# Optimization experiments

Measured on AMD Instinct MI355X. Metric: run time of the kernel, lower is better.

The kernel has to match this reference:

```python
import math
import jax, jax.numpy as jnp
import numpy as np

B, H, T, D = 4, 16, 1024, 64


def setup_inputs() -> dict:
    key0 = jax.random.key(0)
    ks = jax.random.split(key0, 5)
    return {
        "query": jax.random.normal(ks[0], (B, H, T, D), dtype=jnp.float32),
        "key": jax.random.normal(ks[1], (B, H, T, D), dtype=jnp.float32),
        "value": jax.random.normal(ks[2], (B, H, T, D), dtype=jnp.float32),
        "edges_key": jax.random.normal(ks[3], (T, T, D), dtype=jnp.float32),
        "edges_value": jax.random.normal(ks[4], (T, T, D), dtype=jnp.float32),
        "mask": jnp.ones((B, 1, 1, T), dtype=bool),
    }


def reference(query, key, value, edges_key, edges_value, mask):
    d = query.shape[-1]
    # content-content scores [B,H,T,T]
    scores = jnp.einsum("bhqd,bhkd->bhqk", query, key)
    # content-position scores via relative edge keys [T,T,D]
    scores = scores + jnp.einsum("bhqd,qkd->bhqk", query, edges_key)
    scores = scores * (1.0 / math.sqrt(d))
    scores = jnp.where(mask, scores, jnp.float32(-1e9))
    a = jax.nn.softmax(scores, axis=-1)  # dropout is identity in eval / pdrop=0
    # value update + relative edge-value update
    out = jnp.einsum("bhqk,bhkd->bhqd", a, value)
    out = out + jnp.einsum("bhqk,qkd->bhqd", a, edges_value)
    return out
```

## Files before the change

### kernel.cpp

```cpp
#include <hip/hip_runtime.h>

#define Tt 1024
#define Dh 64
#define SCALE 0.125f

typedef __attribute__((ext_vector_type(4))) float f32x4;
typedef __attribute__((ext_vector_type(8))) short bf16x8;

__device__ inline unsigned short f2bf(float x){
  unsigned u = __float_as_uint(x);
  unsigned r = (u + 0x7FFFu + ((u >> 16) & 1u)) >> 16;
  return (unsigned short)r;
}
__device__ inline float bf2f(unsigned short h){
  return __uint_as_float(((unsigned)h) << 16);
}
__device__ inline ushort4 pack4(float4 f){
  ushort4 u; u.x=f2bf(f.x); u.y=f2bf(f.y); u.z=f2bf(f.z); u.w=f2bf(f.w); return u;
}
__device__ inline bf16x8 pack8(float4 a, float4 b){
  bf16x8 r;
  r[0]=(short)f2bf(a.x); r[1]=(short)f2bf(a.y); r[2]=(short)f2bf(a.z); r[3]=(short)f2bf(a.w);
  r[4]=(short)f2bf(b.x); r[5]=(short)f2bf(b.y); r[6]=(short)f2bf(b.z); r[7]=(short)f2bf(b.w);
  return r;
}
__device__ inline f32x4 mfma16(bf16x8 a, bf16x8 b, f32x4 c){
  return __builtin_amdgcn_mfma_f32_16x16x32_bf16(a, b, c, 0, 0, 0);
}

__device__ inline void stage64x64(const float* __restrict__ g, unsigned short (*lds)[68], int tid){
  int r = tid >> 2, c = (tid & 3) * 16;
  const float4* g4 = (const float4*)(g + (size_t)r * 64 + c);
  float4 f0 = g4[0], f1 = g4[1], f2_ = g4[2], f3 = g4[3];
  ushort4* d4 = (ushort4*)&lds[r][c];
  d4[0]=pack4(f0); d4[1]=pack4(f1); d4[2]=pack4(f2_); d4[3]=pack4(f3);
}
__device__ inline void stage64x64T4(const float* __restrict__ g, unsigned short (*lds)[68], int tid){
  const int kb = (tid >> 4) * 4, db = (tid & 15) * 4;
  float fv[4][4];
#pragma unroll
  for (int j = 0; j < 4; ++j){
    float4 f = *(const float4*)(g + (size_t)(kb + j) * 64 + db);
    fv[j][0]=f.x; fv[j][1]=f.y; fv[j][2]=f.z; fv[j][3]=f.w;
  }
#pragma unroll
  for (int i = 0; i < 4; ++i){
    ushort4 u;
    u.x=f2bf(fv[0][i]); u.y=f2bf(fv[1][i]); u.z=f2bf(fv[2][i]); u.w=f2bf(fv[3][i]);
    *(ushort4*)&lds[db + i][kb] = u;
  }
}
__device__ inline void stage_rows(const unsigned short* __restrict__ g, size_t rowstride,
                                  unsigned short (*lds)[68], int tid){
  int r = tid >> 2, c = (tid & 3) * 16;
  const ushort4* s4 = (const ushort4*)(g + (size_t)r * rowstride + c);
  ushort4 u0=s4[0], u1=s4[1], u2=s4[2], u3=s4[3];
  ushort4* d4 = (ushort4*)&lds[r][c];
  d4[0]=u0; d4[1]=u1; d4[2]=u2; d4[3]=u3;
}
__device__ inline bf16x8 ldsfrag(const unsigned short (*lds)[68], int row, int col){
  const ushort4* p = (const ushort4*)&lds[row][col];
  ushort4 u0 = p[0], u1 = p[1];
  bf16x8 r;
  r[0]=(short)u0.x; r[1]=(short)u0.y; r[2]=(short)u0.z; r[3]=(short)u0.w;
  r[4]=(short)u1.x; r[5]=(short)u1.y; r[6]=(short)u1.z; r[7]=(short)u1.w;
  return r;
}
__device__ inline float fragsum(bf16x8 v){
  float s = 0.f;
#pragma unroll
  for (int i = 0; i < 8; ++i) s += bf2f((unsigned short)v[i]);
  return s;
}

__global__ __launch_bounds__(256) void k_qek(const float* __restrict__ Q,
                                             const float* __restrict__ EK,
                                             unsigned short* __restrict__ BIAS){
  __shared__ unsigned short ek[2][64][68];
  __shared__ unsigned short ot[4][16][68];
  const int qi = blockIdx.x;
  const int tid = threadIdx.x;
  const int w = tid >> 6, l = tid & 63, lr = l & 15, lg = l >> 4;

  bf16x8 a0, a1;
  {
    const float4* q4 = (const float4*)(Q + ((size_t)(16*w + lr) * Tt + qi) * Dh);
    a0 = pack8(q4[lg*2],     q4[lg*2 + 1]);
    a1 = pack8(q4[8 + lg*2], q4[8 + lg*2 + 1]);
  }
  const float* ekq = EK + (size_t)qi * Tt * Dh;
  const int r = l >> 2, c2 = (l & 3) * 16;
  unsigned short* dst0 = BIAS + (size_t)(16*w + r) * Tt * Tt + (size_t)qi * Tt + c2;

  stage64x64(ekq, ek[0], tid);
  __syncthreads();

  for (int kt = 0; kt < 16; ++kt){
    if (kt < 15) stage64x64(ekq + (size_t)(kt+1) * 64 * Dh, ek[(kt+1)&1], tid);
    const unsigned short (*cur)[68] = ek[kt&1];
    f32x4 acc[4];
#pragma unroll
    for (int c = 0; c < 4; ++c){
      bf16x8 b0 = ldsfrag(cur, c*16 + lr, lg*8);
      bf16x8 b1 = ldsfrag(cur, c*16 + lr, lg*8 + 32);
      f32x4 z = {0.f,0.f,0.f,0.f};
      z = mfma16(a0, b0, z);
      z = mfma16(a1, b1, z);
      acc[c] = z;
    }
#pragma unroll
    for (int c = 0; c < 4; ++c)
#pragma unroll
      for (int j = 0; j < 4; ++j)
        ot[w][lg*4 + j][c*16 + lr] = f2bf(acc[c][j]);
    __builtin_amdgcn_wave_barrier();
    {
      const ushort4* s4 = (const ushort4*)&ot[w][r][c2];
      ushort4 u0=s4[0], u1=s4[1], u2=s4[2], u3=s4[3];
      ushort4* d4 = (ushort4*)(dst0 + kt*64);
      d4[0]=u0; d4[1]=u1; d4[2]=u2; d4[3]=u3;
    }
    __builtin_amdgcn_wave_barrier();
    __syncthreads();
  }
}

__global__ __launch_bounds__(256) void k_attn(const float* __restrict__ Q,
                                              const float* __restrict__ K,
                                              const float* __restrict__ V,
                                              unsigned short* WS,
                                              float* __restrict__ OUT){
  __shared__ unsigned short kt_[64][68];
  __shared__ unsigned short bt[64][68];
  __shared__ unsigned short pt[64][68];
  __shared__ unsigned short vt[64][68];
  const int bid = blockIdx.x;
  const int bh = (bid & 7) + ((bid >> 7) << 3);
  const int qt = ((bid >> 3) & 15) * 64;
  const int tid = threadIdx.x;
  const int w = tid >> 6, l = tid & 63, lr = l & 15, lg = l >> 4;

  bf16x8 a0, a1;
  {
    const float4* q4 = (const float4*)(Q + ((size_t)bh * Tt + qt + 16*w + lr) * Dh);
    a0 = pack8(q4[lg*2],     q4[lg*2 + 1]);
    a1 = pack8(q4[8 + lg*2], q4[8 + lg*2 + 1]);
  }
  const float* kb = K + (size_t)bh * Tt * Dh;
  const float* vb = V + (size_t)bh * Tt * Dh;
  unsigned short* wsb = WS + (size_t)bh * Tt * Tt;

  float lsum[4] = {0.f,0.f,0.f,0.f};
  f32x4 oacc[4];
#pragma unroll
  for (int c = 0; c < 4; ++c) oacc[c] = (f32x4){0.f,0.f,0.f,0.f};

  for (int kt = 0; kt < 16; ++kt){
    stage64x64(kb + (size_t)kt * 64 * Dh, kt_, tid);
    stage_rows(wsb + (size_t)qt * Tt + kt*64, Tt, bt, tid);
    stage64x64T4(vb + (size_t)kt * 64 * Dh, vt, tid);
    __syncthreads();
#pragma unroll
    for (int c = 0; c < 4; ++c){
      bf16x8 b0 = ldsfrag(kt_, c*16 + lr, lg*8);
      bf16x8 b1 = ldsfrag(kt_, c*16 + lr, lg*8 + 32);
      f32x4 z = {0.f,0.f,0.f,0.f};
      z = mfma16(a0, b0, z);
      z = mfma16(a1, b1, z);
      int kl = c*16 + lr;
#pragma unroll
      for (int j = 0; j < 4; ++j){
        float s = (z[j] + bf2f(bt[16*w + lg*4 + j][kl])) * SCALE;
        float p = __expf(s);
        lsum[j] += p;
        pt[16*w + lg*4 + j][kl] = f2bf(p);
      }
    }
    __syncthreads();
    {
      int r = tid >> 2, c2 = (tid & 3) * 16;
      const ushort4* s4 = (const ushort4*)&pt[r][c2];
      ushort4 u0=s4[0], u1=s4[1], u2=s4[2], u3=s4[3];
      ushort4* d4 = (ushort4*)(wsb + (size_t)(qt + r) * Tt + kt*64 + c2);
      d4[0]=u0; d4[1]=u1; d4[2]=u2; d4[3]=u3;
    }
    bf16x8 p0 = ldsfrag(pt, 16*w + lr, lg*8);
    bf16x8 p1 = ldsfrag(pt, 16*w + lr, lg*8 + 32);
#pragma unroll
    for (int c = 0; c < 4; ++c){
      bf16x8 v0 = ldsfrag(vt, c*16 + lr, lg*8);
      bf16x8 v1 = ldsfrag(vt, c*16 + lr, lg*8 + 32);
      oacc[c] = mfma16(p0, v0, oacc[c]);
      oacc[c] = mfma16(p1, v1, oacc[c]);
    }
    __syncthreads();
  }
  float rl[4];
#pragma unroll
  for (int j = 0; j < 4; ++j){
    float su = lsum[j];
    for (int o = 1; o < 16; o <<= 1) su += __shfl_xor(su, o, 64);
    rl[j] = 1.f / su;
  }
#pragma unroll
  for (int c = 0; c < 4; ++c)
#pragma unroll
    for (int j = 0; j < 4; ++j)
      OUT[((size_t)bh * Tt + qt + 16*w + lg*4 + j) * Dh + c*16 + lr] = oacc[c][j] * rl[j];
}

__global__ __launch_bounds__(256) void k_aev(const unsigned short* __restrict__ WS,
                                             const float* __restrict__ EV,
                                             float* __restrict__ OUT){
  __shared__ unsigned short evt[2][64][68];
  __shared__ float sums[64];
  const int qi = blockIdx.x;
  const int tid = threadIdx.x;
  const int w = tid >> 6, l = tid & 63, lr = l & 15, lg = l >> 4;

  const unsigned short* arow = WS + (size_t)(16*w + lr) * Tt * Tt + (size_t)qi * Tt;
  const float* evq = EV + (size_t)qi * Tt * Dh;

  f32x4 acc[4];
#pragma unroll
  for (int c = 0; c < 4; ++c) acc[c] = (f32x4){0.f,0.f,0.f,0.f};
  float asum = 0.f;

  stage64x64T4(evq, evt[0], tid);
  __syncthreads();

  for (int kt = 0; kt < 16; ++kt){
    if (kt < 15) stage64x64T4(evq + (size_t)(kt+1) * 64 * Dh, evt[(kt+1)&1], tid);
    const unsigned short (*cur)[68] = evt[kt&1];
    bf16x8 a0 = *(const bf16x8*)(arow + kt*64 + lg*8);
    bf16x8 a1 = *(const bf16x8*)(arow + kt*64 + 32 + lg*8);
    asum += fragsum(a0) + fragsum(a1);
#pragma unroll
    for (int c = 0; c < 4; ++c){
      bf16x8 b0 = ldsfrag(cur, c*16 + lr, lg*8);
      bf16x8 b1 = ldsfrag(cur, c*16 + lr, lg*8 + 32);
      acc[c] = mfma16(a0, b0, acc[c]);
      acc[c] = mfma16(a1, b1, acc[c]);
    }
    __syncthreads();
  }
  asum += __shfl_xor(asum, 16, 64);
  asum += __shfl_xor(asum, 32, 64);
  if (lg == 0) sums[16*w + lr] = asum;
  __builtin_amdgcn_wave_barrier();

#pragma unroll
  for (int c = 0; c < 4; ++c)
#pragma unroll
    for (int j = 0; j < 4; ++j){
      int bh = 16*w + lg*4 + j;
      float rl = 1.f / sums[bh];
      size_t idx = ((size_t)bh * Tt + qi) * Dh + c*16 + lr;
      OUT[idx] += acc[c][j] * rl;
    }
}

extern "C" void kernel_launch(void* const* d_in, const int* in_sizes, int n_in,
                              void* d_out, int out_size, void* d_ws, size_t ws_size,
                              hipStream_t stream){
  const float* Q  = (const float*)d_in[0];
  const float* K  = (const float*)d_in[1];
  const float* V  = (const float*)d_in[2];
  const float* EK = (const float*)d_in[3];
  const float* EV = (const float*)d_in[4];
  float* OUT = (float*)d_out;
  unsigned short* WS = (unsigned short*)d_ws;

  if (ws_size < (size_t)64 * Tt * Tt * sizeof(unsigned short)) return;

  k_qek <<<dim3(1024), dim3(256), 0, stream>>>(Q, EK, WS);
  k_attn<<<dim3(1024), dim3(256), 0, stream>>>(Q, K, V, WS, OUT);
  k_aev <<<dim3(1024), dim3(256), 0, stream>>>(WS, EV, OUT);
}
```

Measured before the change: 267.5 us.

## Register-prefetch next tiles across all three kernels to overlap global loads with MFMA

Splits each LDS staging step into a global-load phase into registers and a later convert-and-store-to-LDS phase, so the next tile's loads are issued before the current tile's MFMA work in k_qek, k_attn and k_aev. k_attn also drops one block barrier by having each wave write back only its own rows of P, and k_aev prefetches the next row of attention probabilities. The fp32-to-bf16 conversion now uses a native __bf16 cast instead of manual rounding. This hides global memory latency at the cost of more live registers, which may lower occupancy.

```diff
diff --git a/kernel.cpp b/kernel.cpp
--- a/kernel.cpp
+++ b/kernel.cpp
@@ -8,9 +8,8 @@
 typedef __attribute__((ext_vector_type(8))) short bf16x8;
 
 __device__ inline unsigned short f2bf(float x){
-  unsigned u = __float_as_uint(x);
-  unsigned r = (u + 0x7FFFu + ((u >> 16) & 1u)) >> 16;
-  return (unsigned short)r;
+  __bf16 h = (__bf16)x;
+  return __builtin_bit_cast(unsigned short, h);
 }
 __device__ inline float bf2f(unsigned short h){
   return __uint_as_float(((unsigned)h) << 16);
@@ -26,37 +25,6 @@
 }
 __device__ inline f32x4 mfma16(bf16x8 a, bf16x8 b, f32x4 c){
   return __builtin_amdgcn_mfma_f32_16x16x32_bf16(a, b, c, 0, 0, 0);
-}
-
-__device__ inline void stage64x64(const float* __restrict__ g, unsigned short (*lds)[68], int tid){
-  int r = tid >> 2, c = (tid & 3) * 16;
-  const float4* g4 = (const float4*)(g + (size_t)r * 64 + c);
-  float4 f0 = g4[0], f1 = g4[1], f2_ = g4[2], f3 = g4[3];
-  ushort4* d4 = (ushort4*)&lds[r][c];
-  d4[0]=pack4(f0); d4[1]=pack4(f1); d4[2]=pack4(f2_); d4[3]=pack4(f3);
-}
-__device__ inline void stage64x64T4(const float* __restrict__ g, unsigned short (*lds)[68], int tid){
-  const int kb = (tid >> 4) * 4, db = (tid & 15) * 4;
-  float fv[4][4];
-#pragma unroll
-  for (int j = 0; j < 4; ++j){
-    float4 f = *(const float4*)(g + (size_t)(kb + j) * 64 + db);
-    fv[j][0]=f.x; fv[j][1]=f.y; fv[j][2]=f.z; fv[j][3]=f.w;
-  }
-#pragma unroll
-  for (int i = 0; i < 4; ++i){
-    ushort4 u;
-    u.x=f2bf(fv[0][i]); u.y=f2bf(fv[1][i]); u.z=f2bf(fv[2][i]); u.w=f2bf(fv[3][i]);
-    *(ushort4*)&lds[db + i][kb] = u;
-  }
-}
-__device__ inline void stage_rows(const unsigned short* __restrict__ g, size_t rowstride,
-                                  unsigned short (*lds)[68], int tid){
-  int r = tid >> 2, c = (tid & 3) * 16;
-  const ushort4* s4 = (const ushort4*)(g + (size_t)r * rowstride + c);
-  ushort4 u0=s4[0], u1=s4[1], u2=s4[2], u3=s4[3];
-  ushort4* d4 = (ushort4*)&lds[r][c];
-  d4[0]=u0; d4[1]=u1; d4[2]=u2; d4[3]=u3;
 }
 __device__ inline bf16x8 ldsfrag(const unsigned short (*lds)[68], int row, int col){
   const ushort4* p = (const ushort4*)&lds[row][col];
@@ -81,6 +49,8 @@
   const int qi = blockIdx.x;
   const int tid = threadIdx.x;
   const int w = tid >> 6, l = tid & 63, lr = l & 15, lg = l >> 4;
+  const int sr = tid >> 2, sc = (tid & 3) * 16;
+  const int or_ = l >> 2, oc = (l & 3) * 16;
 
   bf16x8 a0, a1;
   {
@@ -89,14 +59,23 @@
     a1 = pack8(q4[8 + lg*2], q4[8 + lg*2 + 1]);
   }
   const float* ekq = EK + (size_t)qi * Tt * Dh;
-  const int r = l >> 2, c2 = (l & 3) * 16;
-  unsigned short* dst0 = BIAS + (size_t)(16*w + r) * Tt * Tt + (size_t)qi * Tt + c2;
-
-  stage64x64(ekq, ek[0], tid);
+  unsigned short* dst0 = BIAS + (size_t)(16*w + or_) * Tt * Tt + (size_t)qi * Tt + oc;
+
+  float4 ereg[4];
+  auto issueE = [&](int kt){
+    const float4* g4 = (const float4*)(ekq + (size_t)kt*64*Dh + (size_t)sr*64 + sc);
+    ereg[0]=g4[0]; ereg[1]=g4[1]; ereg[2]=g4[2]; ereg[3]=g4[3];
+  };
+  auto writeE = [&](int buf){
+    ushort4* d4 = (ushort4*)&ek[buf][sr][sc];
+    d4[0]=pack4(ereg[0]); d4[1]=pack4(ereg[1]); d4[2]=pack4(ereg[2]); d4[3]=pack4(ereg[3]);
+  };
+
+  issueE(0); writeE(0);
   __syncthreads();
 
   for (int kt = 0; kt < 16; ++kt){
-    if (kt < 15) stage64x64(ekq + (size_t)(kt+1) * 64 * Dh, ek[(kt+1)&1], tid);
+    if (kt < 15) issueE(kt+1);
     const unsigned short (*cur)[68] = ek[kt&1];
     f32x4 acc[4];
 #pragma unroll
@@ -115,12 +94,13 @@
         ot[w][lg*4 + j][c*16 + lr] = f2bf(acc[c][j]);
     __builtin_amdgcn_wave_barrier();
     {
-      const ushort4* s4 = (const ushort4*)&ot[w][r][c2];
+      const ushort4* s4 = (const ushort4*)&ot[w][or_][oc];
       ushort4 u0=s4[0], u1=s4[1], u2=s4[2], u3=s4[3];
       ushort4* d4 = (ushort4*)(dst0 + kt*64);
       d4[0]=u0; d4[1]=u1; d4[2]=u2; d4[3]=u3;
     }
     __builtin_amdgcn_wave_barrier();
+    if (kt < 15) writeE((kt+1)&1);
     __syncthreads();
   }
 }
@@ -139,6 +119,9 @@
   const int qt = ((bid >> 3) & 15) * 64;
   const int tid = threadIdx.x;
   const int w = tid >> 6, l = tid & 63, lr = l & 15, lg = l >> 4;
+  const int sr = tid >> 2, sc = (tid & 3) * 16;
+  const int vkb = (tid >> 4) * 4, vdb = (tid & 15) * 4;
+  const int or_ = l >> 2, oc = (l & 3) * 16;
 
   bf16x8 a0, a1;
   {
@@ -150,16 +133,43 @@
   const float* vb = V + (size_t)bh * Tt * Dh;
   unsigned short* wsb = WS + (size_t)bh * Tt * Tt;
 
+  float4 kreg[4]; ushort4 breg[4]; float vr[4][4];
+  auto issue = [&](int kt){
+    const float4* kg = (const float4*)(kb + (size_t)kt*64*Dh + (size_t)sr*64 + sc);
+    kreg[0]=kg[0]; kreg[1]=kg[1]; kreg[2]=kg[2]; kreg[3]=kg[3];
+    const ushort4* bg = (const ushort4*)(wsb + (size_t)(qt + sr)*Tt + (size_t)kt*64 + sc);
+    breg[0]=bg[0]; breg[1]=bg[1]; breg[2]=bg[2]; breg[3]=bg[3];
+    const float* vg = vb + (size_t)kt*64*Dh;
+#pragma unroll
+    for (int j = 0; j < 4; ++j){
+      float4 f = *(const float4*)(vg + (size_t)(vkb + j)*64 + vdb);
+      vr[j][0]=f.x; vr[j][1]=f.y; vr[j][2]=f.z; vr[j][3]=f.w;
+    }
+  };
+  auto writeLDS = [&](){
+    ushort4* kd = (ushort4*)&kt_[sr][sc];
+    kd[0]=pack4(kreg[0]); kd[1]=pack4(kreg[1]); kd[2]=pack4(kreg[2]); kd[3]=pack4(kreg[3]);
+    ushort4* bd = (ushort4*)&bt[sr][sc];
+    bd[0]=breg[0]; bd[1]=breg[1]; bd[2]=breg[2]; bd[3]=breg[3];
+#pragma unroll
+    for (int i = 0; i < 4; ++i){
+      ushort4 u;
+      u.x=f2bf(vr[0][i]); u.y=f2bf(vr[1][i]); u.z=f2bf(vr[2][i]); u.w=f2bf(vr[3][i]);
+      *(ushort4*)&vt[vdb + i][vkb] = u;
+    }
+  };
+
   float lsum[4] = {0.f,0.f,0.f,0.f};
   f32x4 oacc[4];
 #pragma unroll
   for (int c = 0; c < 4; ++c) oacc[c] = (f32x4){0.f,0.f,0.f,0.f};
 
+  issue(0);
   for (int kt = 0; kt < 16; ++kt){
-    stage64x64(kb + (size_t)kt * 64 * Dh, kt_, tid);
-    stage_rows(wsb + (size_t)qt * Tt + kt*64, Tt, bt, tid);
-    stage64x64T4(vb + (size_t)kt * 64 * Dh, vt, tid);
     __syncthreads();
+    writeLDS();
+    __syncthreads();
+    if (kt < 15) issue(kt+1);
 #pragma unroll
     for (int c = 0; c < 4; ++c){
       bf16x8 b0 = ldsfrag(kt_, c*16 + lr, lg*8);
@@ -176,12 +186,11 @@
         pt[16*w + lg*4 + j][kl] = f2bf(p);
       }
     }
-    __syncthreads();
+    __builtin_amdgcn_wave_barrier();
     {
-      int r = tid >> 2, c2 = (tid & 3) * 16;
-      const ushort4* s4 = (const ushort4*)&pt[r][c2];
+      const ushort4* s4 = (const ushort4*)&pt[16*w + or_][oc];
       ushort4 u0=s4[0], u1=s4[1], u2=s4[2], u3=s4[3];
-      ushort4* d4 = (ushort4*)(wsb + (size_t)(qt + r) * Tt + kt*64 + c2);
+      ushort4* d4 = (ushort4*)(wsb + (size_t)(qt + 16*w + or_)*Tt + kt*64 + oc);
       d4[0]=u0; d4[1]=u1; d4[2]=u2; d4[3]=u3;
     }
     bf16x8 p0 = ldsfrag(pt, 16*w + lr, lg*8);
@@ -193,7 +202,6 @@
       oacc[c] = mfma16(p0, v0, oacc[c]);
       oacc[c] = mfma16(p1, v1, oacc[c]);
     }
-    __syncthreads();
   }
   float rl[4];
 #pragma unroll
@@ -217,30 +225,58 @@
   const int qi = blockIdx.x;
   const int tid = threadIdx.x;
   const int w = tid >> 6, l = tid & 63, lr = l & 15, lg = l >> 4;
+  const int vkb = (tid >> 4) * 4, vdb = (tid & 15) * 4;
 
   const unsigned short* arow = WS + (size_t)(16*w + lr) * Tt * Tt + (size_t)qi * Tt;
   const float* evq = EV + (size_t)qi * Tt * Dh;
 
+  float vr[4][4];
+  auto issueEV = [&](int kt){
+    const float* vg = evq + (size_t)kt*64*Dh;
+#pragma unroll
+    for (int j = 0; j < 4; ++j){
+      float4 f = *(const float4*)(vg + (size_t)(vkb + j)*64 + vdb);
+      vr[j][0]=f.x; vr[j][1]=f.y; vr[j][2]=f.z; vr[j][3]=f.w;
+    }
+  };
+  auto writeEV = [&](int buf){
+#pragma unroll
+    for (int i = 0; i < 4; ++i){
+      ushort4 u;
+      u.x=f2bf(vr[0][i]); u.y=f2bf(vr[1][i]); u.z=f2bf(vr[2][i]); u.w=f2bf(vr[3][i]);
+      *(ushort4*)&evt[buf][vdb + i][vkb] = u;
+    }
+  };
+
   f32x4 acc[4];
 #pragma unroll
   for (int c = 0; c < 4; ++c) acc[c] = (f32x4){0.f,0.f,0.f,0.f};
   float asum = 0.f;
 
-  stage64x64T4(evq, evt[0], tid);
+  issueEV(0); writeEV(0);
+  bf16x8 pa0 = *(const bf16x8*)(arow + lg*8);
+  bf16x8 pa1 = *(const bf16x8*)(arow + 32 + lg*8);
   __syncthreads();
 
   for (int kt = 0; kt < 16; ++kt){
-    if (kt < 15) stage64x64T4(evq + (size_t)(kt+1) * 64 * Dh, evt[(kt+1)&1], tid);
+    bf16x8 na0, na1;
+    if (kt < 15){
+      issueEV(kt+1);
+      na0 = *(const bf16x8*)(arow + (kt+1)*64 + lg*8);
+      na1 = *(const bf16x8*)(arow + (kt+1)*64 + 32 + lg*8);
+    }
+    asum += fragsum(pa0) + fragsum(pa1);
     const unsigned short (*cur)[68] = evt[kt&1];
-    bf16x8 a0 = *(const bf16x8*)(arow + kt*64 + lg*8);
-    bf16x8 a1 = *(const bf16x8*)(arow + kt*64 + 32 + lg*8);
-    asum += fragsum(a0) + fragsum(a1);
 #pragma unroll
     for (int c = 0; c < 4; ++c){
       bf16x8 b0 = ldsfrag(cur, c*16 + lr, lg*8);
       bf16x8 b1 = ldsfrag(cur, c*16 + lr, lg*8 + 32);
-      acc[c] = mfma16(a0, b0, acc[c]);
-      acc[c] = mfma16(a1, b1, acc[c]);
+      acc[c] = mfma16(pa0, b0, acc[c]);
+      acc[c] = mfma16(pa1, b1, acc[c]);
+    }
+    if (kt < 15){
+      writeEV((kt+1)&1);
+      pa0 = na0; pa1 = na1;
     }
     __syncthreads();
   }
```

After: 286.1 us. 7.0% more time.

## Store bias in per-thread fragment layout and double-buffer K/V tiles in attention

Applied to the files above, without the earlier changes.

The edge-key bias kernel now writes its bf16 scores straight from registers into a layout where each attention thread can load its 16 bias values with two vector loads. This removes the LDS transpose in k_qek and the LDS staging of bias in k_attn. k_attn double-buffers the K and V tiles and prefetches the next bias fragment, so one block-wide barrier per tile is replaced by a wave barrier. The 1/sqrt(d) scale is folded into Q. The bias and the probabilities now live in separate workspace buffers, which doubles the workspace requirement, and f2bf uses the native bf16 conversion.

```diff
diff --git a/kernel.cpp b/kernel.cpp
--- a/kernel.cpp
+++ b/kernel.cpp
@@ -2,15 +2,14 @@
 
 #define Tt 1024
 #define Dh 64
-#define SCALE 0.125f
 
 typedef __attribute__((ext_vector_type(4))) float f32x4;
 typedef __attribute__((ext_vector_type(8))) short bf16x8;
+typedef __attribute__((ext_vector_type(8))) unsigned short u16x8;
 
 __device__ inline unsigned short f2bf(float x){
-  unsigned u = __float_as_uint(x);
-  unsigned r = (u + 0x7FFFu + ((u >> 16) & 1u)) >> 16;
-  return (unsigned short)r;
+  __bf16 h = (__bf16)x;
+  return __builtin_bit_cast(unsigned short, h);
 }
 __device__ inline float bf2f(unsigned short h){
   return __uint_as_float(((unsigned)h) << 16);
@@ -49,14 +48,6 @@
     u.x=f2bf(fv[0][i]); u.y=f2bf(fv[1][i]); u.z=f2bf(fv[2][i]); u.w=f2bf(fv[3][i]);
     *(ushort4*)&lds[db + i][kb] = u;
   }
-}
-__device__ inline void stage_rows(const unsigned short* __restrict__ g, size_t rowstride,
-                                  unsigned short (*lds)[68], int tid){
-  int r = tid >> 2, c = (tid & 3) * 16;
-  const ushort4* s4 = (const ushort4*)(g + (size_t)r * rowstride + c);
-  ushort4 u0=s4[0], u1=s4[1], u2=s4[2], u3=s4[3];
-  ushort4* d4 = (ushort4*)&lds[r][c];
-  d4[0]=u0; d4[1]=u1; d4[2]=u2; d4[3]=u3;
 }
 __device__ inline bf16x8 ldsfrag(const unsigned short (*lds)[68], int row, int col){
   const ushort4* p = (const ushort4*)&lds[row][col];
@@ -75,28 +66,39 @@
 
 __global__ __launch_bounds__(256) void k_qek(const float* __restrict__ Q,
                                              const float* __restrict__ EK,
-                                             unsigned short* __restrict__ BIAS){
+                                             unsigned short* __restrict__ BIASF){
   __shared__ unsigned short ek[2][64][68];
-  __shared__ unsigned short ot[4][16][68];
-  const int qi = blockIdx.x;
+  const int bid = blockIdx.x;
+  const int qi = (bid >> 3) + 128 * (bid & 7);
   const int tid = threadIdx.x;
   const int w = tid >> 6, l = tid & 63, lr = l & 15, lg = l >> 4;
 
   bf16x8 a0, a1;
   {
     const float4* q4 = (const float4*)(Q + ((size_t)(16*w + lr) * Tt + qi) * Dh);
-    a0 = pack8(q4[lg*2],     q4[lg*2 + 1]);
-    a1 = pack8(q4[8 + lg*2], q4[8 + lg*2 + 1]);
+    float4 qa=q4[lg*2], qb=q4[lg*2+1], qc=q4[8+lg*2], qd=q4[8+lg*2+1];
+    qa.x*=0.125f; qa.y*=0.125f; qa.z*=0.125f; qa.w*=0.125f;
+    qb.x*=0.125f; qb.y*=0.125f; qb.z*=0.125f; qb.w*=0.125f;
+    qc.x*=0.125f; qc.y*=0.125f; qc.z*=0.125f; qc.w*=0.125f;
+    qd.x*=0.125f; qd.y*=0.125f; qd.z*=0.125f; qd.w*=0.125f;
+    a0 = pack8(qa, qb); a1 = pack8(qc, qd);
   }
   const float* ekq = EK + (size_t)qi * Tt * Dh;
-  const int r = l >> 2, c2 = (l & 3) * 16;
-  unsigned short* dst0 = BIAS + (size_t)(16*w + r) * Tt * Tt + (size_t)qi * Tt + c2;
+  const int qt2 = qi >> 6, J = qi & 3;
+  const int tid2 = ((qi >> 4) & 3) * 64 + ((qi >> 2) & 3) * 16 + lr;
+  size_t sb[4];
+#pragma unroll
+  for (int j = 0; j < 4; ++j){
+    int bh = 16*w + 4*lg + j;
+    sb[j] = (size_t)(bh*16 + qt2) * 65536 + (size_t)tid2 * 16 + J * 4;
+  }
 
   stage64x64(ekq, ek[0], tid);
   __syncthreads();
 
+#pragma unroll 2
   for (int kt = 0; kt < 16; ++kt){
-    if (kt < 15) stage64x64(ekq + (size_t)(kt+1) * 64 * Dh, ek[(kt+1)&1], tid);
+    if (kt < 15) stage64x64(ekq + (size_t)(kt+1)*64*Dh, ek[(kt+1)&1], tid);
     const unsigned short (*cur)[68] = ek[kt&1];
     f32x4 acc[4];
 #pragma unroll
@@ -109,18 +111,11 @@
       acc[c] = z;
     }
 #pragma unroll
-    for (int c = 0; c < 4; ++c)
-#pragma unroll
-      for (int j = 0; j < 4; ++j)
-        ot[w][lg*4 + j][c*16 + lr] = f2bf(acc[c][j]);
-    __builtin_amdgcn_wave_barrier();
-    {
-      const ushort4* s4 = (const ushort4*)&ot[w][r][c2];
-      ushort4 u0=s4[0], u1=s4[1], u2=s4[2], u3=s4[3];
-      ushort4* d4 = (ushort4*)(dst0 + kt*64);
-      d4[0]=u0; d4[1]=u1; d4[2]=u2; d4[3]=u3;
-    }
-    __builtin_amdgcn_wave_barrier();
+    for (int j = 0; j < 4; ++j){
+      ushort4 u;
+      u.x=f2bf(acc[0][j]); u.y=f2bf(acc[1][j]); u.z=f2bf(acc[2][j]); u.w=f2bf(acc[3][j]);
+      *(ushort4*)(BIASF + sb[j] + (size_t)kt * 4096) = u;
+    }
     __syncthreads();
   }
 }
@@ -128,71 +123,90 @@
 __global__ __launch_bounds__(256) void k_attn(const float* __restrict__ Q,
                                               const float* __restrict__ K,
                                               const float* __restrict__ V,
-                                              unsigned short* WS,
+                                              const unsigned short* __restrict__ BIASF,
+                                              unsigned short* __restrict__ P,
                                               float* __restrict__ OUT){
-  __shared__ unsigned short kt_[64][68];
-  __shared__ unsigned short bt[64][68];
+  __shared__ unsigned short ktile[2][64][68];
+  __shared__ unsigned short vtile[2][64][68];
   __shared__ unsigned short pt[64][68];
-  __shared__ unsigned short vt[64][68];
   const int bid = blockIdx.x;
   const int bh = (bid & 7) + ((bid >> 7) << 3);
-  const int qt = ((bid >> 3) & 15) * 64;
+  const int qt2 = (bid >> 3) & 15;
+  const int qt = qt2 * 64;
   const int tid = threadIdx.x;
   const int w = tid >> 6, l = tid & 63, lr = l & 15, lg = l >> 4;
+  const int or_ = l >> 2, oc = (l & 3) * 16;
 
   bf16x8 a0, a1;
   {
     const float4* q4 = (const float4*)(Q + ((size_t)bh * Tt + qt + 16*w + lr) * Dh);
-    a0 = pack8(q4[lg*2],     q4[lg*2 + 1]);
-    a1 = pack8(q4[8 + lg*2], q4[8 + lg*2 + 1]);
+    float4 qa=q4[lg*2], qb=q4[lg*2+1], qc=q4[8+lg*2], qd=q4[8+lg*2+1];
+    qa.x*=0.125f; qa.y*=0.125f; qa.z*=0.125f; qa.w*=0.125f;
+    qb.x*=0.125f; qb.y*=0.125f; qb.z*=0.125f; qb.w*=0.125f;
+    qc.x*=0.125f; qc.y*=0.125f; qc.z*=0.125f; qc.w*=0.125f;
+    qd.x*=0.125f; qd.y*=0.125f; qd.z*=0.125f; qd.w*=0.125f;
+    a0 = pack8(qa, qb); a1 = pack8(qc, qd);
   }
   const float* kb = K + (size_t)bh * Tt * Dh;
   const float* vb = V + (size_t)bh * Tt * Dh;
-  unsigned short* wsb = WS + (size_t)bh * Tt * Tt;
+  unsigned short* pb = P + (size_t)bh * Tt * Tt;
+  const unsigned short* bbase = BIASF + (size_t)(bh*16 + qt2) * 65536 + (size_t)tid * 16;
 
   float lsum[4] = {0.f,0.f,0.f,0.f};
   f32x4 oacc[4];
 #pragma unroll
   for (int c = 0; c < 4; ++c) oacc[c] = (f32x4){0.f,0.f,0.f,0.f};
 
+  u16x8 bc0, bc1, bn0, bn1;
+  stage64x64 (kb, ktile[0], tid);
+  stage64x64T4(vb, vtile[0], tid);
+  { const u16x8* bp = (const u16x8*)bbase; bc0 = bp[0]; bc1 = bp[1]; }
+  __syncthreads();
+
+#pragma unroll 2
   for (int kt = 0; kt < 16; ++kt){
-    stage64x64(kb + (size_t)kt * 64 * Dh, kt_, tid);
-    stage_rows(wsb + (size_t)qt * Tt + kt*64, Tt, bt, tid);
-    stage64x64T4(vb + (size_t)kt * 64 * Dh, vt, tid);
-    __syncthreads();
-#pragma unroll
-    for (int c = 0; c < 4; ++c){
-      bf16x8 b0 = ldsfrag(kt_, c*16 + lr, lg*8);
-      bf16x8 b1 = ldsfrag(kt_, c*16 + lr, lg*8 + 32);
+    if (kt < 15){
+      stage64x64 (kb + (size_t)(kt+1)*64*Dh, ktile[(kt+1)&1], tid);
+      stage64x64T4(vb + (size_t)(kt+1)*64*Dh, vtile[(kt+1)&1], tid);
+      const u16x8* bp = (const u16x8*)(bbase + (size_t)(kt+1) * 4096);
+      bn0 = bp[0]; bn1 = bp[1];
+    }
+    const unsigned short (*kc)[68] = ktile[kt&1];
+    const unsigned short (*vc)[68] = vtile[kt&1];
+#pragma unroll
+    for (int c = 0; c < 4; ++c){
+      bf16x8 b0 = ldsfrag(kc, c*16 + lr, lg*8);
+      bf16x8 b1 = ldsfrag(kc, c*16 + lr, lg*8 + 32);
       f32x4 z = {0.f,0.f,0.f,0.f};
       z = mfma16(a0, b0, z);
       z = mfma16(a1, b1, z);
       int kl = c*16 + lr;
 #pragma unroll
       for (int j = 0; j < 4; ++j){
-        float s = (z[j] + bf2f(bt[16*w + lg*4 + j][kl])) * SCALE;
-        float p = __expf(s);
+        const int idx = j*4 + c;
+        float bv = bf2f(idx < 8 ? bc0[idx] : bc1[idx-8]);
+        float p = __expf(z[j] + bv);
         lsum[j] += p;
         pt[16*w + lg*4 + j][kl] = f2bf(p);
       }
     }
-    __syncthreads();
+    __builtin_amdgcn_wave_barrier();
     {
-      int r = tid >> 2, c2 = (tid & 3) * 16;
-      const ushort4* s4 = (const ushort4*)&pt[r][c2];
+      const ushort4* s4 = (const ushort4*)&pt[16*w + or_][oc];
       ushort4 u0=s4[0], u1=s4[1], u2=s4[2], u3=s4[3];
-      ushort4* d4 = (ushort4*)(wsb + (size_t)(qt + r) * Tt + kt*64 + c2);
+      ushort4* d4 = (ushort4*)(pb + (size_t)(qt + 16*w + or_)*Tt + kt*64 + oc);
       d4[0]=u0; d4[1]=u1; d4[2]=u2; d4[3]=u3;
     }
     bf16x8 p0 = ldsfrag(pt, 16*w + lr, lg*8);
     bf16x8 p1 = ldsfrag(pt, 16*w + lr, lg*8 + 32);
 #pragma unroll
     for (int c = 0; c < 4; ++c){
-      bf16x8 v0 = ldsfrag(vt, c*16 + lr, lg*8);
-      bf16x8 v1 = ldsfrag(vt, c*16 + lr, lg*8 + 32);
+      bf16x8 v0 = ldsfrag(vc, c*16 + lr, lg*8);
+      bf16x8 v1 = ldsfrag(vc, c*16 + lr, lg*8 + 32);
       oacc[c] = mfma16(p0, v0, oacc[c]);
       oacc[c] = mfma16(p1, v1, oacc[c]);
     }
+    bc0 = bn0; bc1 = bn1;
     __syncthreads();
   }
   float rl[4];
@@ -209,7 +223,7 @@
       OUT[((size_t)bh * Tt + qt + 16*w + lg*4 + j) * Dh + c*16 + lr] = oacc[c][j] * rl[j];
 }
 
-__global__ __launch_bounds__(256) void k_aev(const unsigned short* __restrict__ WS,
+__global__ __launch_bounds__(256) void k_aev(const unsigned short* __restrict__ P,
                                              const float* __restrict__ EV,
                                              float* __restrict__ OUT){
   __shared__ unsigned short evt[2][64][68];
@@ -218,7 +232,7 @@
   const int tid = threadIdx.x;
   const int w = tid >> 6, l = tid & 63, lr = l & 15, lg = l >> 4;
 
-  const unsigned short* arow = WS + (size_t)(16*w + lr) * Tt * Tt + (size_t)qi * Tt;
+  const unsigned short* arow = P + (size_t)(16*w + lr) * Tt * Tt + (size_t)qi * Tt;
   const float* evq = EV + (size_t)qi * Tt * Dh;
 
   f32x4 acc[4];
@@ -229,6 +243,7 @@
   stage64x64T4(evq, evt[0], tid);
   __syncthreads();
 
+#pragma unroll 2
   for (int kt = 0; kt < 16; ++kt){
     if (kt < 15) stage64x64T4(evq + (size_t)(kt+1) * 64 * Dh, evt[(kt+1)&1], tid);
     const unsigned short (*cur)[68] = evt[kt&1];
@@ -269,11 +284,12 @@
   const float* EK = (const float*)d_in[3];
   const float* EV = (const float*)d_in[4];
   float* OUT = (float*)d_out;
-  unsigned short* WS = (unsigned short*)d_ws;
-
-  if (ws_size < (size_t)64 * Tt * Tt * sizeof(unsigned short)) return;
-
-  k_qek <<<dim3(1024), dim3(256), 0, stream>>>(Q, EK, WS);
-  k_attn<<<dim3(1024), dim3(256), 0, stream>>>(Q, K, V, WS, OUT);
-  k_aev <<<dim3(1024), dim3(256), 0, stream>>>(WS, EV, OUT);
-}
+  unsigned short* WSP = (unsigned short*)d_ws;
+  unsigned short* WS2 = WSP + (size_t)64 * Tt * Tt;
+
+  if (ws_size < (size_t)2 * 64 * Tt * Tt * sizeof(unsigned short)) return;
+
+  k_qek <<<dim3(1024), dim3(256), 0, stream>>>(Q, EK, WS2);
+  k_attn<<<dim3(1024), dim3(256), 0, stream>>>(Q, K, V, WS2, WSP, OUT);
+  k_aev <<<dim3(1024), dim3(256), 0, stream>>>(WSP, EV, OUT);
+}
```

After: 310.4 us. 16.0% more time.
